# Kernel optimization log

Hardware: AMD Instinct MI355X
Metric: run time of the kernel (lower is better)

The kernel has to match this reference:

```python
import jax, jax.numpy as jnp
import numpy as np

B, CIN, H, W = 2, 3, 768, 768
CB = 32          # backbone out_channels (= channels_mid for heads)
ORDER = 5
MARGIN = 3.0     # ScaledTanh margin of refinement head


def _conv(x, w, b, pad):
    # x: [N,C,H,W], w: [O,I,kh,kw]
    y = jax.lax.conv_general_dilated(x, w, (1, 1), [(pad, pad), (pad, pad)],
                                     dimension_numbers=('NCHW', 'OIHW', 'NCHW'))
    return y + b[None, :, None, None]


def _readout(x, w1, b1, s, t, w2, b2, pad):
    # conv(k) -> batchnorm(eval, folded to scale/shift) -> relu -> dropout(eval=id) -> conv1x1
    h = _conv(x, w1, b1, pad)
    h = jax.nn.relu(h * s[None, :, None, None] + t[None, :, None, None])
    return _conv(h, w2, b2, 0)


def setup_inputs() -> dict:
    key = jax.random.key(0)
    ks = iter(jax.random.split(key, 16))
    def rn(shape, scale=0.05):
        return jax.random.normal(next(ks), shape, jnp.float32) * scale
    d = {'inputs': jax.random.normal(next(ks), (B, CIN, H, W), jnp.float32)}
    d['bb_w'] = rn((CB, CIN, 3, 3)); d['bb_b'] = jnp.zeros((CB,), jnp.float32)
    def head(name, k, cout):
        d[name + '_w1'] = rn((CB, CB, k, k)); d[name + '_b1'] = jnp.zeros((CB,), jnp.float32)
        d[name + '_s'] = jnp.ones((CB,), jnp.float32); d[name + '_t'] = jnp.zeros((CB,), jnp.float32)
        d[name + '_w2'] = rn((cout, CB, 1, 1)); d[name + '_b2'] = jnp.zeros((cout,), jnp.float32)
    head('score', 3, 2)
    head('loc', 7, 2)
    head('four', 7, ORDER * 4)
    head('ref', 7, 2)
    return d


def reference(inputs, bb_w, bb_b,
              score_w1, score_b1, score_s, score_t, score_w2, score_b2,
              loc_w1, loc_b1, loc_s, loc_t, loc_w2, loc_b2,
              four_w1, four_b1, four_s, four_t, four_w2, four_b2,
              ref_w1, ref_b1, ref_s, ref_t, ref_w2, ref_b2):
    # backbone (simple conv + relu; out_channels is an int so contour == refinement features)
    feats = jax.nn.relu(_conv(inputs, bb_w, bb_b, 1))
    scores = _readout(feats, score_w1, score_b1, score_s, score_t, score_w2, score_b2, 1)
    locations = _readout(feats, loc_w1, loc_b1, loc_s, loc_t, loc_w2, loc_b2, 3)
    fourier = _readout(feats, four_w1, four_b1, four_s, four_t, four_w2, four_b2, 3)
    # ReadOut final activation ScaledTanh(3.0), then CPNCore multiplies by internal margin 1.0;
    # feature HW == input HW (stride 1), so F.interpolate is a no-op.
    refinement = jnp.tanh(_readout(feats, ref_w1, ref_b1, ref_s, ref_t, ref_w2, ref_b2, 3)) * MARGIN
    return (scores, locations, refinement, fourier)
```

## Files before the change

### kernel.cpp

```cpp
#include <hip/hip_runtime.h>
#include <hip/hip_bf16.h>
#include <cmath>

#define HH 768
#define WW 768
#define HWSZ (768*768)

typedef __attribute__((ext_vector_type(8))) short bhalf8;
typedef __attribute__((ext_vector_type(4))) float f32x4;
typedef __attribute__((ext_vector_type(16))) float f32x16;

__device__ inline ushort f2bf(float f) {
  __hip_bfloat16 h = __float2bfloat16(f);
  return *reinterpret_cast<ushort*>(&h);
}
__device__ inline float bf2f(ushort u) {
  union { unsigned int i; float f; } v; v.i = ((unsigned int)u) << 16; return v.f;
}

__global__ __launch_bounds__(256) void wxform_all_kernel(
    const float* __restrict__ w1S, const float* __restrict__ b1S,
    const float* __restrict__ sS,  const float* __restrict__ tS,
    const float* __restrict__ w1L, const float* __restrict__ b1L,
    const float* __restrict__ sL,  const float* __restrict__ tL,
    const float* __restrict__ w1F, const float* __restrict__ b1F,
    const float* __restrict__ sF,  const float* __restrict__ tF,
    const float* __restrict__ w1R, const float* __restrict__ b1R,
    const float* __restrict__ sR,  const float* __restrict__ tR,
    ushort* __restrict__ wT0, float* __restrict__ bb0, size_t wt_stride_elems)
{
  int h = blockIdx.y;
  const float *w1, *b1, *s, *t;
  int npos;
  if (h == 0)      { w1 = w1S; b1 = b1S; s = sS; t = tS; npos = 9;  }
  else if (h == 1) { w1 = w1L; b1 = b1L; s = sL; t = tL; npos = 49; }
  else if (h == 2) { w1 = w1F; b1 = b1F; s = sF; t = tF; npos = 49; }
  else             { w1 = w1R; b1 = b1R; s = sR; t = tR; npos = 49; }

  ushort* wT = wT0 + (size_t)h * wt_stride_elems;
  float*  bb = bb0 + h * 32;

  int i = blockIdx.x * 256 + threadIdx.x;
  if (i < npos * 1024) {
    int pos = i >> 10, mc = i & 1023, m = mc >> 5, c = mc & 31;
    wT[i] = f2bf(w1[(m * 32 + c) * npos + pos] * s[m]);
  }
  if (blockIdx.x == 0 && i < 32) bb[i] = b1[i] * s[i] + t[i];
}

__global__ __launch_bounds__(256) void backbone_kernel(
    const float* __restrict__ x, const float* __restrict__ w,
    const float* __restrict__ bias, ushort* __restrict__ feats)
{
  int p = blockIdx.x * 256 + threadIdx.x;
  int bb  = p / HWSZ;
  int rem = p - bb * HWSZ;
  int y   = rem / WW;
  int xx  = rem - y * WW;
  const float* xb = x + (size_t)bb * 3 * HWSZ;

  float v[3][3][3];
  #pragma unroll
  for (int c = 0; c < 3; c++)
    #pragma unroll
    for (int dy = 0; dy < 3; dy++)
      #pragma unroll
      for (int dx = 0; dx < 3; dx++) {
        int yy = y + dy - 1, xq = xx + dx - 1;
        v[c][dy][dx] = (yy >= 0 && yy < HH && xq >= 0 && xq < WW)
                         ? xb[(size_t)c * HWSZ + yy * WW + xq] : 0.f;
      }

  union { ushort u[32]; uint4 q[4]; } pk;
  #pragma unroll
  for (int o = 0; o < 32; o++) {
    float acc = bias[o];
    #pragma unroll
    for (int c = 0; c < 3; c++)
      #pragma unroll
      for (int dy = 0; dy < 3; dy++)
        #pragma unroll
        for (int dx = 0; dx < 3; dx++)
          acc = fmaf(w[((o * 3 + c) * 3 + dy) * 3 + dx], v[c][dy][dx], acc);
    pk.u[o] = f2bf(fmaxf(acc, 0.f));
  }
  uint4* dst = (uint4*)(feats + ((size_t)bb * HWSZ + rem) * 32);
  #pragma unroll
  for (int i = 0; i < 4; i++) dst[i] = pk.q[i];
}

template <int COUT, bool DO_TANH>
__device__ inline void head_epilogue3(
    const f32x16 acc[2], const float* __restrict__ bbh,
    const float* __restrict__ w2, const float* __restrict__ b2,
    float* __restrict__ out_base, ushort* mid,
    int wv, int qr, int qc, int kg, int by, int bx, int bb)
{
  #pragma unroll
  for (int n = 0; n < 2; n++) {
    int px = (2 * wv + qr) * 32 + n * 16 + qc;
    #pragma unroll
    for (int rg = 0; rg < 4; rg++) {
      int m0 = 8 * rg + 4 * kg;
      ushort u[4];
      #pragma unroll
      for (int j = 0; j < 4; j++)
        u[j] = f2bf(fmaxf(acc[n][rg * 4 + j] + bbh[m0 + j], 0.f));
      uint2 pkv;
      pkv.x = (unsigned int)u[0] | ((unsigned int)u[1] << 16);
      pkv.y = (unsigned int)u[2] | ((unsigned int)u[3] << 16);
      *(uint2*)(mid + px * 36 + m0) = pkv;
    }
  }
  __syncthreads();

  int t = threadIdx.x;
  float mv[32];
  #pragma unroll
  for (int j = 0; j < 8; j++) {
    uint2 r = *(const uint2*)(mid + t * 36 + j * 4);
    mv[j * 4 + 0] = bf2f((ushort)(r.x & 0xffff));
    mv[j * 4 + 1] = bf2f((ushort)(r.x >> 16));
    mv[j * 4 + 2] = bf2f((ushort)(r.y & 0xffff));
    mv[j * 4 + 3] = bf2f((ushort)(r.y >> 16));
  }
  int oy = by * 16 + (t >> 5), ox = bx * 32 + (t & 31);
  size_t opix = (size_t)oy * WW + ox;
  float* ob = out_base + (size_t)bb * COUT * HWSZ;
  #pragma unroll
  for (int oc = 0; oc < COUT; oc++) {
    float a2 = b2[oc];
    #pragma unroll
    for (int m = 0; m < 32; m++) a2 = fmaf(w2[oc * 32 + m], mv[m], a2);
    if (DO_TANH) a2 = tanhf(a2) * 3.0f;
    ob[(size_t)oc * HWSZ + opix] = a2;
  }
  __syncthreads();
}

__global__ __launch_bounds__(512, 2) void heads3_kernel(
    const ushort* __restrict__ feats,
    const ushort* __restrict__ wtL, const ushort* __restrict__ wtF,
    const ushort* __restrict__ wtR,
    const float* __restrict__ bbL, const float* __restrict__ bbF,
    const float* __restrict__ bbR,
    const float* __restrict__ w2L, const float* __restrict__ b2L,
    const float* __restrict__ w2F, const float* __restrict__ b2F,
    const float* __restrict__ w2R, const float* __restrict__ b2R,
    float* __restrict__ outL, float* __restrict__ outF, float* __restrict__ outR)
{
  __shared__ __align__(16) char smem[53504 + 2 * 28672];
  ushort* tile  = (ushort*)smem;
  ushort* wrow0 = (ushort*)(smem + 53504);
  ushort* wrow1 = (ushort*)(smem + 53504 + 28672);

  int bx = blockIdx.x % 24;
  int by = (blockIdx.x / 24) % 48;
  int bb = blockIdx.x / 1152;
  int x0 = bx * 32 - 3, y0 = by * 16 - 3;
  const ushort* fB = feats + (size_t)bb * HWSZ * 32;

  for (int p = threadIdx.x; p < 22 * 38; p += 512) {
    int r = p / 38, cl = p - r * 38;
    int yy = y0 + r, xx = x0 + cl;
    uint4 q0 = {0,0,0,0}, q1 = {0,0,0,0}, q2 = {0,0,0,0}, q3 = {0,0,0,0};
    if (yy >= 0 && yy < HH && xx >= 0 && xx < WW) {
      const uint4* src = (const uint4*)(fB + ((size_t)yy * WW + xx) * 32);
      q0 = src[0]; q1 = src[1]; q2 = src[2]; q3 = src[3];
    }
    ushort* dst = tile + r * 1216 + cl * 8;
    *(uint4*)(dst +   0) = q0;
    *(uint4*)(dst + 304) = q1;
    *(uint4*)(dst + 608) = q2;
    *(uint4*)(dst + 912) = q3;
  }

  int tid = threadIdx.x;
  int l  = tid & 63;
  int wv = tid >> 6;
  int q  = l & 31;
  int kg = l >> 5;
  int qr = q >> 4, qc = q & 15;

  const ushort* pb  = tile + (2 * wv + qr) * 1216 + kg * 304 + qc * 8;
  const int aOff = kg * 256 + q * 8;
  const ushort* aGR = wtR + q * 32 + kg * 8;

  const ushort *stp0, *stp1, *stp2, *stp3;
  {
    int c, kx, h, g, m;
    c = tid;         kx = c >> 8; h = (c >> 7) & 1; g = (c >> 5) & 3; m = c & 31;
    stp0 = (h ? wtF : wtL) + kx * 1024 + m * 32 + g * 8;
    c = 512 + tid;   kx = c >> 8; h = (c >> 7) & 1; g = (c >> 5) & 3; m = c & 31;
    stp1 = (h ? wtF : wtL) + kx * 1024 + m * 32 + g * 8;
    c = 1024 + tid;  kx = c >> 8; h = (c >> 7) & 1; g = (c >> 5) & 3; m = c & 31;
    stp2 = (h ? wtF : wtL) + kx * 1024 + m * 32 + g * 8;
    c = 1536 + tid;  kx = c >> 8; h = (c >> 7) & 1; g = (c >> 5) & 3; m = c & 31;
    stp3 = (h ? wtF : wtL) + kx * 1024 + m * 32 + g * 8;
  }
  const bool st3 = (tid < 256);

  {
    bhalf8 v0 = *(const bhalf8*)(stp0);
    bhalf8 v1 = *(const bhalf8*)(stp1);
    bhalf8 v2 = *(const bhalf8*)(stp2);
    *(bhalf8*)(wrow0 + (size_t)tid * 8) = v0;
    *(bhalf8*)(wrow0 + (size_t)(512 + tid) * 8) = v1;
    *(bhalf8*)(wrow0 + (size_t)(1024 + tid) * 8) = v2;
    if (st3) {
      bhalf8 v3 = *(const bhalf8*)(stp3);
      *(bhalf8*)(wrow0 + (size_t)(1536 + tid) * 8) = v3;
    }
  }
  __syncthreads();

  f32x16 accL[2] = {};
  f32x16 accF[2] = {};
  f32x16 accR[2] = {};

  #pragma unroll 1
  for (int ky = 0; ky < 7; ky++) {
    ushort* bufR = (ky & 1) ? wrow1 : wrow0;
    ushort* bufW = (ky & 1) ? wrow0 : wrow1;
    const ushort* aB = bufR + aOff;
    const ushort* aR = aGR + ky * 7168;
    const ushort* pbrow = pb + ky * 1216;

    bhalf8 pB0, pB1, pB2, pB3;
    if (ky < 6) {
      pB0 = *(const bhalf8*)(stp0 + (ky + 1) * 7168);
      pB1 = *(const bhalf8*)(stp1 + (ky + 1) * 7168);
      pB2 = *(const bhalf8*)(stp2 + (ky + 1) * 7168);
      if (st3) pB3 = *(const bhalf8*)(stp3 + (ky + 1) * 7168);
    }

    bhalf8 fR[7][2];
    #pragma unroll
    for (int kx = 0; kx < 2; kx++) {
      fR[kx][0] = *(const bhalf8*)(aR + kx * 1024);
      fR[kx][1] = *(const bhalf8*)(aR + kx * 1024 + 16);
    }

    bhalf8 cL0 = *(const bhalf8*)(aB);
    bhalf8 cL1 = *(const bhalf8*)(aB + 512);
    bhalf8 cF0 = *(const bhalf8*)(aB + 1024);
    bhalf8 cF1 = *(const bhalf8*)(aB + 1536);
    bhalf8 cB00 = *(const bhalf8*)(pbrow);
    bhalf8 cB01 = *(const bhalf8*)(pbrow + 608);
    bhalf8 cB10 = *(const bhalf8*)(pbrow + 128);
    bhalf8 cB11 = *(const bhalf8*)(pbrow + 608 + 128);

    #pragma unroll
    for (int kx = 0; kx < 7; kx++) {
      bhalf8 nL0, nL1, nF0, nF1, nB00, nB01, nB10, nB11;
      if (kx < 6) {
        const ushort* a2 = aB + (kx + 1) * 2048;
        nL0 = *(const bhalf8*)(a2);
        nL1 = *(const bhalf8*)(a2 + 512);
        nF0 = *(const bhalf8*)(a2 + 1024);
        nF1 = *(const bhalf8*)(a2 + 1536);
        const ushort* p2 = pbrow + (kx + 1) * 8;
        nB00 = *(const bhalf8*)(p2);
        nB01 = *(const bhalf8*)(p2 + 608);
        nB10 = *(const bhalf8*)(p2 + 128);
        nB11 = *(const bhalf8*)(p2 + 608 + 128);
      }
      if (kx + 2 < 7) {
        fR[kx + 2][0] = *(const bhalf8*)(aR + (kx + 2) * 1024);
        fR[kx + 2][1] = *(const bhalf8*)(aR + (kx + 2) * 1024 + 16);
      }

      __builtin_amdgcn_s_setprio(1);
      accL[0] = __builtin_amdgcn_mfma_f32_32x32x16_bf16(cL0, cB00, accL[0], 0, 0, 0);
      accL[1] = __builtin_amdgcn_mfma_f32_32x32x16_bf16(cL0, cB10, accL[1], 0, 0, 0);
      accF[0] = __builtin_amdgcn_mfma_f32_32x32x16_bf16(cF0, cB00, accF[0], 0, 0, 0);
      accF[1] = __builtin_amdgcn_mfma_f32_32x32x16_bf16(cF0, cB10, accF[1], 0, 0, 0);
      accR[0] = __builtin_amdgcn_mfma_f32_32x32x16_bf16(fR[kx][0], cB00, accR[0], 0, 0, 0);
      accR[1] = __builtin_amdgcn_mfma_f32_32x32x16_bf16(fR[kx][0], cB10, accR[1], 0, 0, 0);
      accL[0] = __builtin_amdgcn_mfma_f32_32x32x16_bf16(cL1, cB01, accL[0], 0, 0, 0);
      accL[1] = __builtin_amdgcn_mfma_f32_32x32x16_bf16(cL1, cB11, accL[1], 0, 0, 0);
      accF[0] = __builtin_amdgcn_mfma_f32_32x32x16_bf16(cF1, cB01, accF[0], 0, 0, 0);
      accF[1] = __builtin_amdgcn_mfma_f32_32x32x16_bf16(cF1, cB11, accF[1], 0, 0, 0);
      accR[0] = __builtin_amdgcn_mfma_f32_32x32x16_bf16(fR[kx][1], cB01, accR[0], 0, 0, 0);
      accR[1] = __builtin_amdgcn_mfma_f32_32x32x16_bf16(fR[kx][1], cB11, accR[1], 0, 0, 0);
      __builtin_amdgcn_s_setprio(0);

      if (kx < 6) {
        cL0 = nL0; cL1 = nL1; cF0 = nF0; cF1 = nF1;
        cB00 = nB00; cB01 = nB01; cB10 = nB10; cB11 = nB11;
      }
    }

    if (ky < 6) {
      *(bhalf8*)(bufW + (size_t)tid * 8) = pB0;
      *(bhalf8*)(bufW + (size_t)(512 + tid) * 8) = pB1;
      *(bhalf8*)(bufW + (size_t)(1024 + tid) * 8) = pB2;
      if (st3) *(bhalf8*)(bufW + (size_t)(1536 + tid) * 8) = pB3;
    }
    __syncthreads();
  }

  ushort* mid = (ushort*)smem;

  head_epilogue3<2,  false>(accL, bbL, w2L, b2L, outL, mid, wv, qr, qc, kg, by, bx, bb);
  head_epilogue3<20, false>(accF, bbF, w2F, b2F, outF, mid, wv, qr, qc, kg, by, bx, bb);
  head_epilogue3<2,  true >(accR, bbR, w2R, b2R, outR, mid, wv, qr, qc, kg, by, bx, bb);
}

template <int COUT, bool DO_TANH>
__device__ inline void head_epilogue_s(
    const f32x16 acc[2], const float* __restrict__ bbh,
    const float* __restrict__ w2, const float* __restrict__ b2,
    float* __restrict__ out_base, float* mid,
    int wv, int qr, int qc, int kg, int by, int bx, int bb)
{
  #pragma unroll
  for (int n = 0; n < 2; n++) {
    int pix = (wv * 4 + 2 * n + qr) * 16 + qc;
    #pragma unroll
    for (int rg = 0; rg < 4; rg++) {
      int m0 = 8 * rg + 4 * kg;
      f32x4 v;
      #pragma unroll
      for (int j = 0; j < 4; j++)
        v[j] = fmaxf(acc[n][rg * 4 + j] + bbh[m0 + j], 0.f);
      *(f32x4*)(mid + pix * 36 + m0) = v;
    }
  }
  __syncthreads();

  int t = threadIdx.x;
  float mv[32];
  #pragma unroll
  for (int j2 = 0; j2 < 8; j2++)
    *(f32x4*)(mv + 4 * j2) = *(const f32x4*)(mid + t * 36 + 4 * j2);

  int oy = by * 16 + (t >> 4), ox = bx * 16 + (t & 15);
  size_t opix = (size_t)oy * WW + ox;
  float* ob = out_base + (size_t)bb * COUT * HWSZ;
  #pragma unroll
  for (int oc = 0; oc < COUT; oc++) {
    float a2 = b2[oc];
    #pragma unroll
    for (int m = 0; m < 32; m++) a2 = fmaf(w2[oc * 32 + m], mv[m], a2);
    if (DO_TANH) a2 = tanhf(a2) * 3.0f;
    ob[(size_t)oc * HWSZ + opix] = a2;
  }
}

__global__ __launch_bounds__(256, 4) void score_kernel(
    const ushort* __restrict__ feats,
    const ushort* __restrict__ wtS, const float* __restrict__ bbS,
    const float* __restrict__ w2S, const float* __restrict__ b2S,
    float* __restrict__ outS)
{
  constexpr int TW = 18, CPAD = 40;
  constexpr int SMEM_BYTES = 256 * 36 * 4;
  __shared__ __align__(16) char smem[SMEM_BYTES];
  ushort* tile = (ushort*)smem;

  int bx = blockIdx.x % 48;
  int by = (blockIdx.x / 48) % 48;
  int bb = blockIdx.x / 2304;
  int x0 = bx * 16 - 1, y0 = by * 16 - 1;
  const ushort* fB = feats + (size_t)bb * HWSZ * 32;

  for (int p = threadIdx.x; p < TW * TW; p += 256) {
    int py = p / TW, pxx = p % TW;
    int yy = y0 + py, xx = x0 + pxx;
    uint4 q0 = {0,0,0,0}, q1 = {0,0,0,0}, q2 = {0,0,0,0}, q3 = {0,0,0,0};
    if (yy >= 0 && yy < HH && xx >= 0 && xx < WW) {
      const uint4* src = (const uint4*)(fB + ((size_t)yy * WW + xx) * 32);
      q0 = src[0]; q1 = src[1]; q2 = src[2]; q3 = src[3];
    }
    uint4* dst = (uint4*)(tile + (size_t)p * CPAD);
    dst[0] = q0; dst[1] = q1; dst[2] = q2; dst[3] = q3;
  }
  __syncthreads();

  int l  = threadIdx.x & 63;
  int wv = threadIdx.x >> 6;
  int q  = l & 31;
  int kg = l >> 5;
  int qr = q >> 4, qc = q & 15;

  const ushort* pb = tile + ((wv * 4 + qr) * TW + qc) * CPAD + kg * 8;
  const int aoff = q * 32 + kg * 8;

  f32x16 acc[2] = {};

  #pragma unroll
  for (int ky = 0; ky < 3; ky++) {
    #pragma unroll
    for (int kx = 0; kx < 3; kx++) {
      const int tap = ky * 3 + kx;
      bhalf8 a0[2];
      #pragma unroll
      for (int kh = 0; kh < 2; kh++)
        a0[kh] = *(const bhalf8*)(wtS + tap * 1024 + aoff + kh * 16);
      #pragma unroll
      for (int n = 0; n < 2; n++) {
        #pragma unroll
        for (int kh = 0; kh < 2; kh++) {
          bhalf8 bf = *(const bhalf8*)(pb + (ky * TW + kx) * CPAD
                                          + n * 2 * TW * CPAD + kh * 16);
          acc[n] = __builtin_amdgcn_mfma_f32_32x32x16_bf16(a0[kh], bf, acc[n], 0, 0, 0);
        }
      }
    }
  }

  __syncthreads();
  float* mid = (float*)smem;
  head_epilogue_s<2, false>(acc, bbS, w2S, b2S, outS, mid, wv, qr, qc, kg, by, bx, bb);
}

extern "C" void kernel_launch(void* const* d_in, const int* in_sizes, int n_in,
                              void* d_out, int out_size, void* d_ws, size_t ws_size,
                              hipStream_t stream) {
  const float* input = (const float*)d_in[0];
  const float* bb_w  = (const float*)d_in[1];
  const float* bb_b  = (const float*)d_in[2];

  ushort* feats = (ushort*)d_ws;
  char* base = (char*)d_ws;
  const size_t FEATS_BYTES = (size_t)2 * HWSZ * 32 * 2;
  const size_t WT_STRIDE_E = 49 * 1024;
  ushort* wT0 = (ushort*)(base + FEATS_BYTES);
  float*  bb0 = (float*)(base + FEATS_BYTES + 4 * WT_STRIDE_E * 2);
  (void)out_size; (void)ws_size; (void)n_in; (void)in_sizes;

  float* out = (float*)d_out;
  float* outS = out;
  float* outL = out + (size_t)4  * HWSZ;
  float* outR = out + (size_t)8  * HWSZ;
  float* outF = out + (size_t)12 * HWSZ;

  dim3 wxgrid(196, 4);
  wxform_all_kernel<<<wxgrid, 256, 0, stream>>>(
      (const float*)d_in[3],  (const float*)d_in[4],  (const float*)d_in[5],  (const float*)d_in[6],
      (const float*)d_in[9],  (const float*)d_in[10], (const float*)d_in[11], (const float*)d_in[12],
      (const float*)d_in[15], (const float*)d_in[16], (const float*)d_in[17], (const float*)d_in[18],
      (const float*)d_in[21], (const float*)d_in[22], (const float*)d_in[23], (const float*)d_in[24],
      wT0, bb0, WT_STRIDE_E);

  backbone_kernel<<<4608, 256, 0, stream>>>(input, bb_w, bb_b, feats);

  const ushort* wtS = wT0 + 0 * WT_STRIDE_E;
  const ushort* wtL = wT0 + 1 * WT_STRIDE_E;
  const ushort* wtF = wT0 + 2 * WT_STRIDE_E;
  const ushort* wtR = wT0 + 3 * WT_STRIDE_E;

  heads3_kernel<<<2 * 48 * 24, 512, 0, stream>>>(
      feats, wtL, wtF, wtR,
      bb0 + 32, bb0 + 64, bb0 + 96,
      (const float*)d_in[13], (const float*)d_in[14],
      (const float*)d_in[19], (const float*)d_in[20],
      (const float*)d_in[25], (const float*)d_in[26],
      outL, outF, outR);

  score_kernel<<<2 * 48 * 48, 256, 0, stream>>>(
      feats, wtS, bb0 + 0,
      (const float*)d_in[7], (const float*)d_in[8], outS);
}
```

Before: 414.8 us.

## Fuse 3x3 score head into the 7x7 heads kernel, reusing its feature tile

Drops the separate score_kernel and computes the 3x3 score conv inside the heads kernel, using the feature tile already held in shared memory. The score MFMAs run after the 7x7 loop and before the remaining epilogues, with staging moved to the weight-buffer region so the tile stays intact. This removes one launch and a second full read of the feature map. The cost is more register pressure and a longer serial tail in the heads kernel.

```diff
diff --git a/kernel.cpp b/kernel.cpp
--- a/kernel.cpp
+++ b/kernel.cpp
@@ -138,16 +138,18 @@
   __syncthreads();
 }
 
-__global__ __launch_bounds__(512, 2) void heads3_kernel(
+__global__ __launch_bounds__(512, 2) void heads4_kernel(
     const ushort* __restrict__ feats,
-    const ushort* __restrict__ wtL, const ushort* __restrict__ wtF,
-    const ushort* __restrict__ wtR,
-    const float* __restrict__ bbL, const float* __restrict__ bbF,
-    const float* __restrict__ bbR,
+    const ushort* __restrict__ wtS, const ushort* __restrict__ wtL,
+    const ushort* __restrict__ wtF, const ushort* __restrict__ wtR,
+    const float* __restrict__ bbS, const float* __restrict__ bbL,
+    const float* __restrict__ bbF, const float* __restrict__ bbR,
+    const float* __restrict__ w2S, const float* __restrict__ b2S,
     const float* __restrict__ w2L, const float* __restrict__ b2L,
     const float* __restrict__ w2F, const float* __restrict__ b2F,
     const float* __restrict__ w2R, const float* __restrict__ b2R,
-    float* __restrict__ outL, float* __restrict__ outF, float* __restrict__ outR)
+    float* __restrict__ outS, float* __restrict__ outL,
+    float* __restrict__ outF, float* __restrict__ outR)
 {
   __shared__ __align__(16) char smem[53504 + 2 * 28672];
   ushort* tile  = (ushort*)smem;
@@ -185,6 +187,7 @@
   const ushort* pb  = tile + (2 * wv + qr) * 1216 + kg * 304 + qc * 8;
   const int aOff = kg * 256 + q * 8;
   const ushort* aGR = wtR + q * 32 + kg * 8;
+  const ushort* aGS = wtS + q * 32 + kg * 8;
 
   const ushort *stp0, *stp1, *stp2, *stp3;
   {
@@ -300,119 +303,41 @@
     __syncthreads();
   }
 
-  ushort* mid = (ushort*)smem;
-
-  head_epilogue3<2,  false>(accL, bbL, w2L, b2L, outL, mid, wv, qr, qc, kg, by, bx, bb);
+  ushort* mid = (ushort*)(smem + 53504);
+
+  head_epilogue3<2, false>(accL, bbL, w2L, b2L, outL, mid, wv, qr, qc, kg, by, bx, bb);
+
+  {
+    f32x16 accS[2] = {};
+    bhalf8 fS[9][2];
+    #pragma unroll
+    for (int t9 = 0; t9 < 2; t9++) {
+      fS[t9][0] = *(const bhalf8*)(aGS + t9 * 1024);
+      fS[t9][1] = *(const bhalf8*)(aGS + t9 * 1024 + 16);
+    }
+    const ushort* pbS = pb + 2 * 1216 + 2 * 8;
+    #pragma unroll
+    for (int t9 = 0; t9 < 9; t9++) {
+      const int sy = t9 / 3, sx = t9 % 3;
+      if (t9 + 2 < 9) {
+        fS[t9 + 2][0] = *(const bhalf8*)(aGS + (t9 + 2) * 1024);
+        fS[t9 + 2][1] = *(const bhalf8*)(aGS + (t9 + 2) * 1024 + 16);
+      }
+      const ushort* p2 = pbS + sy * 1216 + sx * 8;
+      bhalf8 b00 = *(const bhalf8*)(p2);
+      bhalf8 b01 = *(const bhalf8*)(p2 + 608);
+      bhalf8 b10 = *(const bhalf8*)(p2 + 128);
+      bhalf8 b11 = *(const bhalf8*)(p2 + 608 + 128);
+      accS[0] = __builtin_amdgcn_mfma_f32_32x32x16_bf16(fS[t9][0], b00, accS[0], 0, 0, 0);
+      accS[1] = __builtin_amdgcn_mfma_f32_32x32x16_bf16(fS[t9][0], b10, accS[1], 0, 0, 0);
+      accS[0] = __builtin_amdgcn_mfma_f32_32x32x16_bf16(fS[t9][1], b01, accS[0], 0, 0, 0);
+      accS[1] = __builtin_amdgcn_mfma_f32_32x32x16_bf16(fS[t9][1], b11, accS[1], 0, 0, 0);
+    }
+    head_epilogue3<2, false>(accS, bbS, w2S, b2S, outS, mid, wv, qr, qc, kg, by, bx, bb);
+  }
+
   head_epilogue3<20, false>(accF, bbF, w2F, b2F, outF, mid, wv, qr, qc, kg, by, bx, bb);
   head_epilogue3<2,  true >(accR, bbR, w2R, b2R, outR, mid, wv, qr, qc, kg, by, bx, bb);
-}
-
-template <int COUT, bool DO_TANH>
-__device__ inline void head_epilogue_s(
-    const f32x16 acc[2], const float* __restrict__ bbh,
-    const float* __restrict__ w2, const float* __restrict__ b2,
-    float* __restrict__ out_base, float* mid,
-    int wv, int qr, int qc, int kg, int by, int bx, int bb)
-{
-  #pragma unroll
-  for (int n = 0; n < 2; n++) {
-    int pix = (wv * 4 + 2 * n + qr) * 16 + qc;
-    #pragma unroll
-    for (int rg = 0; rg < 4; rg++) {
-      int m0 = 8 * rg + 4 * kg;
-      f32x4 v;
-      #pragma unroll
-      for (int j = 0; j < 4; j++)
-        v[j] = fmaxf(acc[n][rg * 4 + j] + bbh[m0 + j], 0.f);
-      *(f32x4*)(mid + pix * 36 + m0) = v;
-    }
-  }
-  __syncthreads();
-
-  int t = threadIdx.x;
-  float mv[32];
-  #pragma unroll
-  for (int j2 = 0; j2 < 8; j2++)
-    *(f32x4*)(mv + 4 * j2) = *(const f32x4*)(mid + t * 36 + 4 * j2);
-
-  int oy = by * 16 + (t >> 4), ox = bx * 16 + (t & 15);
-  size_t opix = (size_t)oy * WW + ox;
-  float* ob = out_base + (size_t)bb * COUT * HWSZ;
-  #pragma unroll
-  for (int oc = 0; oc < COUT; oc++) {
-    float a2 = b2[oc];
-    #pragma unroll
-    for (int m = 0; m < 32; m++) a2 = fmaf(w2[oc * 32 + m], mv[m], a2);
-    if (DO_TANH) a2 = tanhf(a2) * 3.0f;
-    ob[(size_t)oc * HWSZ + opix] = a2;
-  }
-}
-
-__global__ __launch_bounds__(256, 4) void score_kernel(
-    const ushort* __restrict__ feats,
-    const ushort* __restrict__ wtS, const float* __restrict__ bbS,
-    const float* __restrict__ w2S, const float* __restrict__ b2S,
-    float* __restrict__ outS)
-{
-  constexpr int TW = 18, CPAD = 40;
-  constexpr int SMEM_BYTES = 256 * 36 * 4;
-  __shared__ __align__(16) char smem[SMEM_BYTES];
-  ushort* tile = (ushort*)smem;
-
-  int bx = blockIdx.x % 48;
-  int by = (blockIdx.x / 48) % 48;
-  int bb = blockIdx.x / 2304;
-  int x0 = bx * 16 - 1, y0 = by * 16 - 1;
-  const ushort* fB = feats + (size_t)bb * HWSZ * 32;
-
-  for (int p = threadIdx.x; p < TW * TW; p += 256) {
-    int py = p / TW, pxx = p % TW;
-    int yy = y0 + py, xx = x0 + pxx;
-    uint4 q0 = {0,0,0,0}, q1 = {0,0,0,0}, q2 = {0,0,0,0}, q3 = {0,0,0,0};
-    if (yy >= 0 && yy < HH && xx >= 0 && xx < WW) {
-      const uint4* src = (const uint4*)(fB + ((size_t)yy * WW + xx) * 32);
-      q0 = src[0]; q1 = src[1]; q2 = src[2]; q3 = src[3];
-    }
-    uint4* dst = (uint4*)(tile + (size_t)p * CPAD);
-    dst[0] = q0; dst[1] = q1; dst[2] = q2; dst[3] = q3;
-  }
-  __syncthreads();
-
-  int l  = threadIdx.x & 63;
-  int wv = threadIdx.x >> 6;
-  int q  = l & 31;
-  int kg = l >> 5;
-  int qr = q >> 4, qc = q & 15;
-
-  const ushort* pb = tile + ((wv * 4 + qr) * TW + qc) * CPAD + kg * 8;
-  const int aoff = q * 32 + kg * 8;
-
-  f32x16 acc[2] = {};
-
-  #pragma unroll
-  for (int ky = 0; ky < 3; ky++) {
-    #pragma unroll
-    for (int kx = 0; kx < 3; kx++) {
-      const int tap = ky * 3 + kx;
-      bhalf8 a0[2];
-      #pragma unroll
-      for (int kh = 0; kh < 2; kh++)
-        a0[kh] = *(const bhalf8*)(wtS + tap * 1024 + aoff + kh * 16);
-      #pragma unroll
-      for (int n = 0; n < 2; n++) {
-        #pragma unroll
-        for (int kh = 0; kh < 2; kh++) {
-          bhalf8 bf = *(const bhalf8*)(pb + (ky * TW + kx) * CPAD
-                                          + n * 2 * TW * CPAD + kh * 16);
-          acc[n] = __builtin_amdgcn_mfma_f32_32x32x16_bf16(a0[kh], bf, acc[n], 0, 0, 0);
-        }
-      }
-    }
-  }
-
-  __syncthreads();
-  float* mid = (float*)smem;
-  head_epilogue_s<2, false>(acc, bbS, w2S, b2S, outS, mid, wv, qr, qc, kg, by, bx, bb);
 }
 
 extern "C" void kernel_launch(void* const* d_in, const int* in_sizes, int n_in,
@@ -451,15 +376,12 @@
   const ushort* wtF = wT0 + 2 * WT_STRIDE_E;
   const ushort* wtR = wT0 + 3 * WT_STRIDE_E;
 
-  heads3_kernel<<<2 * 48 * 24, 512, 0, stream>>>(
-      feats, wtL, wtF, wtR,
-      bb0 + 32, bb0 + 64, bb0 + 96,
+  heads4_kernel<<<2 * 48 * 24, 512, 0, stream>>>(
+      feats, wtS, wtL, wtF, wtR,
+      bb0 + 0, bb0 + 32, bb0 + 64, bb0 + 96,
+      (const float*)d_in[7],  (const float*)d_in[8],
       (const float*)d_in[13], (const float*)d_in[14],
       (const float*)d_in[19], (const float*)d_in[20],
       (const float*)d_in[25], (const float*)d_in[26],
-      outL, outF, outR);
-
-  score_kernel<<<2 * 48 * 48, 256, 0, stream>>>(
-      feats, wtS, bb0 + 0,
-      (const float*)d_in[7], (const float*)d_in[8], outS);
-}
+      outS, outL, outF, outR);
+}
```

After: 415.2 us. About the same (+0.1%).
